# Performance work log

Measured on AMD Instinct MI355X. Metric: run time of the kernel, lower is better.

The kernel has to match this reference:

```python
import jax, jax.numpy as jnp
import numpy as np

B, S, D, V = 64, 128, 64, 50000

def _prelu(x, a):
    return jnp.where(x >= 0, x, a * x)

def setup_inputs() -> dict:
    key = jax.random.key(0)
    ks = jax.random.split(key, 24)
    stdv = 1.0 / np.sqrt(D)
    u = lambda k, shape: jax.random.uniform(k, shape, jnp.float32, -stdv, stdv)
    emb = u(ks[0], (V, D)).at[0].set(0.0)  # padding_idx=0
    inp = {
        'items': jax.random.randint(ks[1], (B, S), 0, V),
        'A': jax.random.randint(ks[2], (B, S, S), 0, 2),
        'edgeorder': jax.random.randint(ks[3], (B, S, S), 0, S),
        'last_nodes': jax.random.randint(ks[4], (B,), 0, S),
        'mask': jnp.ones((B, S), dtype=bool),
        'emb': emb,
        'W_self': u(ks[5], (D, D)), 'W_neigh': u(ks[6], (D, D)),
        'prelu1': jnp.full((D,), 0.25, jnp.float32),
        'Wq': u(ks[7], (D, D)), 'bq': jnp.zeros((D,), jnp.float32),
        'Wk': u(ks[8], (D, D)), 'Wv': u(ks[9], (D, D)), 'we': u(ks[10], (D,)),
        'prelu2': jnp.full((D,), 0.25, jnp.float32),
        'Wu': u(ks[11], (D, D)), 'bu': jnp.zeros((D,), jnp.float32),
        'Wvr': u(ks[12], (D, D)), 'wer': u(ks[13], (D,)),
        'prelu3': jnp.full((D,), 0.25, jnp.float32),
        'W_sr': u(ks[14], (2 * D, D)),
    }
    return inp

def reference(items, A, edgeorder, last_nodes, mask, emb, W_self, W_neigh, prelu1,
              Wq, bq, Wk, Wv, we, prelu2, Wu, bu, Wvr, wer, prelu3, W_sr):
    x = emb[items]  # [B,S,D]
    # ---- EOPA: masked neighbor broadcast + edgeorder gather + max-pool ----
    adjT = (jnp.swapaxes(A, 1, 2) == 1)  # [B,S(target),S(neighbor)]
    neigh = jnp.where((adjT & mask[:, None, :])[..., None], x[:, None, :, :], 0.0)  # [B,S,S,D]
    eo_t = jnp.swapaxes(edgeorder, 1, 2)  # [B,S,S]
    # gathered[b,i,j,:] = neigh[b, edgeorder[b,j,i], j, :]
    neigh = jnp.take_along_axis(neigh, eo_t[..., None], axis=1)
    neigh = neigh.max(axis=2)  # [B,S,D]
    h = _prelu(x @ W_self + neigh @ W_neigh, prelu1)
    # ---- SGAT: sigmoid-gated attention over adjacency ----
    q = h @ Wq + bq
    k = h @ Wk
    v = h @ Wv
    e = k[:, :, None, :] + q[:, None, :, :]             # e[b,i,j,d]
    e = jnp.where((A == 1)[..., None], e, 0.0)
    e = jax.nn.sigmoid(e) @ we                           # [B,S,S]
    a = jax.nn.softmax(e, axis=1)                        # softmax over source i
    h2 = _prelu(jnp.einsum('bij,bid->bjd', a, v), prelu2)
    # ---- AttnReadout ----
    xu = h2 @ Wu + bu                                    # [B,S,D]
    xlast = h2[jnp.arange(h2.shape[0]), last_nodes]      # [B,D]
    xv = xlast @ Wvr
    eatt = jax.nn.sigmoid(xu + xv[:, None, :]) @ wer     # [B,S]
    alpha = jax.nn.softmax(eatt, axis=1)
    out = _prelu((h2 * alpha[..., None]).sum(axis=1), prelu3)  # [B,D]
    # ---- session representation ----
    sr = jnp.concatenate([out, xlast], axis=-1) @ W_sr   # [B,D]
    return sr
```

## Files before the change

### kernel.cpp

```cpp
#include <hip/hip_runtime.h>

#define BB 64
#define SS 128
#define DD 64
#define SSQ (SS*SS)
#define BSD (BB*SS*DD)

__device__ __forceinline__ float fast_sigmoid(float x) {
  return __builtin_amdgcn_rcpf(1.0f + __expf(-x));
}
__device__ __forceinline__ float rl(float v, int l) {
  return __int_as_float(__builtin_amdgcn_readlane(__float_as_int(v), l));
}

__global__ __launch_bounds__(256, 4) void kA(
    const int* __restrict__ items, const int* __restrict__ Aadj,
    const int* __restrict__ eo, const float* __restrict__ emb,
    const float* __restrict__ Wself, const float* __restrict__ Wneigh,
    const float* __restrict__ prelu1,
    const float* __restrict__ Wq, const float* __restrict__ bq,
    const float* __restrict__ Wk, const float* __restrict__ Wv,
    float* __restrict__ q_ws, float* __restrict__ k_ws, float* __restrict__ v_ws)
{
  __shared__ alignas(16) float xs[SS*DD];
  __shared__ unsigned char condw[SS];
  const int b  = blockIdx.x >> 4;
  const int i0 = (blockIdx.x & 15) * 8;
  const int tid = threadIdx.x;
  const int wv = tid >> 6, lane = tid & 63;

  {
    const float4* emb4 = (const float4*)emb;
    float4* xs4 = (float4*)xs;
    for (int f = tid; f < SS*16; f += 256) {
      int j = f >> 4, qd = f & 15;
      xs4[f] = emb4[items[b*SS + j]*16 + qd];
    }
  }
  {
    int eov[4];
#pragma unroll
    for (int kq = 0; kq < 4; kq++) {
      int p = tid + kq*256;
      eov[kq] = eo[b*SSQ + (p >> 3)*SS + i0 + (p & 7)];
    }
#pragma unroll
    for (int kq = 0; kq < 4; kq++) {
      int p = tid + kq*256;
      bool c = (Aadj[b*SSQ + (p >> 3)*SS + eov[kq]] == 1);
      unsigned long long bm = __ballot(c);
      if ((lane & 7) == 0)
        condw[p >> 3] = (unsigned char)(bm >> lane);
    }
  }
  __syncthreads();

  float m[2];
#pragma unroll
  for (int t = 0; t < 2; t++) m[t] = -__builtin_inff();
  for (int j = 0; j < SS; j++) {
    unsigned int cw = (unsigned int)condw[j] >> (wv*2);
    float xv = xs[j*DD + lane];
#pragma unroll
    for (int t = 0; t < 2; t++) {
      float val = ((cw >> t) & 1u) ? xv : 0.0f;
      m[t] = fmaxf(m[t], val);
    }
  }
  float xr[2];
#pragma unroll
  for (int t = 0; t < 2; t++) xr[t] = xs[(i0 + wv*2 + t)*DD + lane];

  float acc[2] = {0.0f, 0.0f};
#pragma unroll 8
  for (int kk = 0; kk < DD; kk++) {
    float w = Wself[kk*DD + lane];
#pragma unroll
    for (int t = 0; t < 2; t++) acc[t] = fmaf(rl(xr[t], kk), w, acc[t]);
  }
#pragma unroll 8
  for (int kk = 0; kk < DD; kk++) {
    float w = Wneigh[kk*DD + lane];
#pragma unroll
    for (int t = 0; t < 2; t++) acc[t] = fmaf(rl(m[t], kk), w, acc[t]);
  }
  float hr[2];
  {
    float p1 = prelu1[lane];
#pragma unroll
    for (int t = 0; t < 2; t++) {
      float h = acc[t];
      hr[t] = (h >= 0.0f) ? h : p1*h;
    }
  }

  const int r0g = b*SS + i0 + wv*2;
  {
    float bqv = bq[lane];
    float a2[2] = {bqv, bqv};
#pragma unroll 8
    for (int kk = 0; kk < DD; kk++) {
      float w = Wq[kk*DD + lane];
#pragma unroll
      for (int t = 0; t < 2; t++) a2[t] = fmaf(rl(hr[t], kk), w, a2[t]);
    }
#pragma unroll
    for (int t = 0; t < 2; t++) q_ws[(r0g + t)*DD + lane] = a2[t];
  }
  {
    float a2[2] = {0.0f, 0.0f};
#pragma unroll 8
    for (int kk = 0; kk < DD; kk++) {
      float w = Wk[kk*DD + lane];
#pragma unroll
      for (int t = 0; t < 2; t++) a2[t] = fmaf(rl(hr[t], kk), w, a2[t]);
    }
#pragma unroll
    for (int t = 0; t < 2; t++) k_ws[(r0g + t)*DD + lane] = a2[t];
  }
  {
    float a2[2] = {0.0f, 0.0f};
#pragma unroll 8
    for (int kk = 0; kk < DD; kk++) {
      float w = Wv[kk*DD + lane];
#pragma unroll
      for (int t = 0; t < 2; t++) a2[t] = fmaf(rl(hr[t], kk), w, a2[t]);
    }
#pragma unroll
    for (int t = 0; t < 2; t++) v_ws[(r0g + t)*DD + lane] = a2[t];
  }
}

__global__ __launch_bounds__(256, 4) void kB(
    const int* __restrict__ Aadj,
    const float* __restrict__ q_ws, const float* __restrict__ k_ws,
    const float* __restrict__ v_ws,
    const float* __restrict__ we, const float* __restrict__ prelu2,
    const float* __restrict__ Wu, const float* __restrict__ bu,
    float* __restrict__ h2_ws, float* __restrict__ xu_ws)
{
  __shared__ alignas(16) float ks[SS*65];
  __shared__ alignas(16) float qs[8*65];
  __shared__ alignas(16) float es[8*129];
  __shared__ float wes[DD];
  const int b  = blockIdx.x >> 4;
  const int j0 = (blockIdx.x & 15) * 8;
  const int tid = threadIdx.x;
  const int wv = tid >> 6, lane = tid & 63;

  {
    const float4* k4 = (const float4*)k_ws;
    for (int f = tid; f < 2048; f += 256) {
      int i = f >> 4, d4 = f & 15;
      float4 v = k4[(b*SS + i)*16 + d4];
      float* dst = &ks[i*65 + d4*4];
      dst[0] = v.x; dst[1] = v.y; dst[2] = v.z; dst[3] = v.w;
    }
    const float4* q4 = (const float4*)q_ws;
    if (tid < 128) {
      int jl = tid >> 4, d4 = tid & 15;
      float4 v = q4[(b*SS + j0 + jl)*16 + d4];
      float* dst = &qs[jl*65 + d4*4];
      dst[0] = v.x; dst[1] = v.y; dst[2] = v.z; dst[3] = v.w;
    }
    if (tid < DD) wes[tid] = we[tid];
  }
  float hw = we[lane];
  for (int off = 32; off >= 1; off >>= 1) hw += __shfl_xor(hw, off);
  const float half_sum = 0.5f * hw;
  __syncthreads();

#pragma unroll
  for (int kq = 0; kq < 4; kq++) {
    int p = tid + kq*256;
    int jl = p & 7, i = p >> 3;
    bool isE = (Aadj[b*SSQ + i*SS + j0 + jl] == 1);
    float s = 0.0f;
    for (int d2 = 0; d2 < DD; d2++) {
      float t = ks[i*65 + d2] + qs[jl*65 + d2];
      s = fmaf(wes[d2], fast_sigmoid(t), s);
    }
    es[jl*129 + i] = isE ? s : half_sum;
  }
  __syncthreads();

  float* vs = ks;
  {
    const float4* v4 = (const float4*)v_ws;
    float4* vs4 = (float4*)vs;
    for (int f = tid; f < 2048; f += 256)
      vs4[f] = v4[b*SS*16 + f];
  }
  float a0n[2], a1n[2];
#pragma unroll
  for (int t = 0; t < 2; t++) {
    int jl = wv*2 + t;
    float a0 = es[jl*129 + lane], a1 = es[jl*129 + 64 + lane];
    float mx = fmaxf(a0, a1);
    for (int off = 32; off >= 1; off >>= 1) mx = fmaxf(mx, __shfl_xor(mx, off));
    float p0 = __expf(a0 - mx), p1 = __expf(a1 - mx);
    float sm = p0 + p1;
    for (int off = 32; off >= 1; off >>= 1) sm += __shfl_xor(sm, off);
    float inv = 1.0f / sm;
    a0n[t] = p0 * inv;
    a1n[t] = p1 * inv;
  }
  __syncthreads();

  float acc[2] = {0.0f, 0.0f};
  for (int i = 0; i < 64; i++) {
    float vv = vs[i*DD + lane];
#pragma unroll
    for (int t = 0; t < 2; t++) acc[t] = fmaf(rl(a0n[t], i), vv, acc[t]);
  }
  for (int i = 0; i < 64; i++) {
    float vv = vs[(64 + i)*DD + lane];
#pragma unroll
    for (int t = 0; t < 2; t++) acc[t] = fmaf(rl(a1n[t], i), vv, acc[t]);
  }
  float h2r[2];
  {
    float p2 = prelu2[lane];
#pragma unroll
    for (int t = 0; t < 2; t++) {
      float h2 = acc[t];
      h2r[t] = (h2 >= 0.0f) ? h2 : p2*h2;
      h2_ws[(b*SS + j0 + wv*2 + t)*DD + lane] = h2r[t];
    }
  }
  {
    float buv = bu[lane];
    float a2[2] = {buv, buv};
#pragma unroll 8
    for (int kk = 0; kk < DD; kk++) {
      float w = Wu[kk*DD + lane];
#pragma unroll
      for (int t = 0; t < 2; t++) a2[t] = fmaf(rl(h2r[t], kk), w, a2[t]);
    }
#pragma unroll
    for (int t = 0; t < 2; t++)
      xu_ws[(b*SS + j0 + wv*2 + t)*DD + lane] = a2[t];
  }
}

__global__ __launch_bounds__(512) void k4_readout(
    const float* __restrict__ h2_ws, const float* __restrict__ xu_ws,
    const int* __restrict__ last_nodes,
    const float* __restrict__ Wvr, const float* __restrict__ wer,
    const float* __restrict__ prelu3, const float* __restrict__ Wsr,
    float* __restrict__ out)
{
  __shared__ float xlast[DD], xv[DD], eatt[SS], alpha[SS], outs[DD];
  __shared__ float pools[8*DD];
  const int b = blockIdx.x;
  const int tid = threadIdx.x;
  const int wv = tid >> 6, lane = tid & 63;

  const int ln = last_nodes[b];
  if (tid < DD) xlast[tid] = h2_ws[(b*SS + ln)*DD + tid];
  __syncthreads();
  {
    float s = 0.0f;
#pragma unroll
    for (int r = 0; r < 8; r++) {
      int k2 = wv*8 + r;
      s = fmaf(xlast[k2], Wvr[k2*DD + lane], s);
    }
    pools[wv*DD + lane] = s;
  }
  __syncthreads();
  if (wv == 0) {
    float s = 0.0f;
#pragma unroll
    for (int w = 0; w < 8; w++) s += pools[w*DD + lane];
    xv[lane] = s;
  }
  __syncthreads();
  {
    float werv = wer[lane];
    float xvl = xv[lane];
    for (int j = wv; j < SS; j += 8) {
      float xuv = xu_ws[(b*SS + j)*DD + lane];
      float term = fast_sigmoid(xuv + xvl) * werv;
      for (int off = 32; off >= 1; off >>= 1) term += __shfl_xor(term, off);
      if (lane == 0) eatt[j] = term;
    }
  }
  __syncthreads();
  if (wv == 0) {
    float a0 = eatt[lane], a1 = eatt[64 + lane];
    float mx = fmaxf(a0, a1);
    for (int off = 32; off >= 1; off >>= 1) mx = fmaxf(mx, __shfl_xor(mx, off));
    float p0 = __expf(a0 - mx), p1 = __expf(a1 - mx);
    float sm = p0 + p1;
    for (int off = 32; off >= 1; off >>= 1) sm += __shfl_xor(sm, off);
    float inv = 1.0f / sm;
    alpha[lane]      = p0 * inv;
    alpha[64 + lane] = p1 * inv;
  }
  __syncthreads();
  {
    float part = 0.0f;
    for (int j = wv; j < SS; j += 8)
      part = fmaf(alpha[j], h2_ws[(b*SS + j)*DD + lane], part);
    pools[wv*DD + lane] = part;
  }
  __syncthreads();
  if (wv == 0) {
    float s = 0.0f;
#pragma unroll
    for (int w = 0; w < 8; w++) s += pools[w*DD + lane];
    float p3 = prelu3[lane];
    outs[lane] = (s >= 0.0f) ? s : p3 * s;
  }
  __syncthreads();
  {
    float fs = 0.0f;
#pragma unroll
    for (int r = 0; r < 16; r++) {
      int m2 = wv*16 + r;
      float src = (m2 < DD) ? outs[m2] : xlast[m2 - DD];
      fs = fmaf(src, Wsr[m2*DD + lane], fs);
    }
    pools[wv*DD + lane] = fs;
  }
  __syncthreads();
  if (wv == 0) {
    float s = 0.0f;
#pragma unroll
    for (int w = 0; w < 8; w++) s += pools[w*DD + lane];
    out[b*DD + lane] = s;
  }
}

extern "C" void kernel_launch(void* const* d_in, const int* in_sizes, int n_in,
                              void* d_out, int out_size, void* d_ws, size_t ws_size,
                              hipStream_t stream)
{
  const int* items = (const int*)d_in[0];
  const int* Aadj  = (const int*)d_in[1];
  const int* eo    = (const int*)d_in[2];
  const int* lastn = (const int*)d_in[3];
  const float* emb    = (const float*)d_in[5];
  const float* Wself  = (const float*)d_in[6];
  const float* Wneigh = (const float*)d_in[7];
  const float* p1     = (const float*)d_in[8];
  const float* Wq     = (const float*)d_in[9];
  const float* bq     = (const float*)d_in[10];
  const float* Wk     = (const float*)d_in[11];
  const float* Wv     = (const float*)d_in[12];
  const float* we     = (const float*)d_in[13];
  const float* p2     = (const float*)d_in[14];
  const float* Wu     = (const float*)d_in[15];
  const float* bu     = (const float*)d_in[16];
  const float* Wvr    = (const float*)d_in[17];
  const float* wer    = (const float*)d_in[18];
  const float* p3     = (const float*)d_in[19];
  const float* Wsr    = (const float*)d_in[20];

  float* ws    = (float*)d_ws;
  float* q_ws  = ws;
  float* k_ws  = ws + (size_t)BSD;
  float* v_ws  = ws + (size_t)2*BSD;
  float* h2_ws = ws + (size_t)3*BSD;
  float* xu_ws = ws + (size_t)4*BSD;

  kA<<<BB*16, 256, 0, stream>>>(items, Aadj, eo, emb, Wself, Wneigh, p1,
                                Wq, bq, Wk, Wv, q_ws, k_ws, v_ws);
  kB<<<BB*16, 256, 0, stream>>>(Aadj, q_ws, k_ws, v_ws, we, p2, Wu, bu,
                                h2_ws, xu_ws);
  k4_readout<<<BB, 512, 0, stream>>>(h2_ws, xu_ws, lastn, Wvr, wer, p3, Wsr,
                                     (float*)d_out);
}
```

Measured before the change: 185.6 us.

## Double rows per block and restructure SGAT edge scoring with transposed K tile

Each block in both kernels now handles 16 rows instead of 8, so the embedding and K/V tiles staged per block are reused twice as much and the grid shrinks to 512 blocks. In kB, K is stored transposed in shared memory, the query lives in registers and is broadcast with readlane, and the adjacency mask is packed into ballot bitmasks. Each lane then computes sigmoid scores for two source nodes across four targets, replacing the per-thread strided dot-product loop and the extra shared-memory score buffer. The trade-off is fewer blocks (about two per CU on a large GPU), higher register pressure with the occupancy hint lowered to 2, and the V load now sitting behind an extra barrier.

Measured after the change: 185.4 us. Within noise of the previous version (-0.2%).

```diff
diff --git a/kernel.cpp b/kernel.cpp
--- a/kernel.cpp
+++ b/kernel.cpp
@@ -13,7 +13,7 @@
   return __int_as_float(__builtin_amdgcn_readlane(__float_as_int(v), l));
 }
 
-__global__ __launch_bounds__(256, 4) void kA(
+__global__ __launch_bounds__(256, 2) void kA(
     const int* __restrict__ items, const int* __restrict__ Aadj,
     const int* __restrict__ eo, const float* __restrict__ emb,
     const float* __restrict__ Wself, const float* __restrict__ Wneigh,
@@ -23,9 +23,9 @@
     float* __restrict__ q_ws, float* __restrict__ k_ws, float* __restrict__ v_ws)
 {
   __shared__ alignas(16) float xs[SS*DD];
-  __shared__ unsigned char condw[SS];
-  const int b  = blockIdx.x >> 4;
-  const int i0 = (blockIdx.x & 15) * 8;
+  __shared__ unsigned short condw[SS];
+  const int b  = blockIdx.x >> 3;
+  const int i0 = (blockIdx.x & 7) * 16;
   const int tid = threadIdx.x;
   const int wv = tid >> 6, lane = tid & 63;
 
@@ -38,100 +38,101 @@
     }
   }
   {
-    int eov[4];
-#pragma unroll
-    for (int kq = 0; kq < 4; kq++) {
+    int eov[8];
+#pragma unroll
+    for (int kq = 0; kq < 8; kq++) {
       int p = tid + kq*256;
-      eov[kq] = eo[b*SSQ + (p >> 3)*SS + i0 + (p & 7)];
-    }
-#pragma unroll
-    for (int kq = 0; kq < 4; kq++) {
+      eov[kq] = eo[b*SSQ + (p >> 4)*SS + i0 + (p & 15)];
+    }
+#pragma unroll
+    for (int kq = 0; kq < 8; kq++) {
       int p = tid + kq*256;
-      bool c = (Aadj[b*SSQ + (p >> 3)*SS + eov[kq]] == 1);
+      bool c = (Aadj[b*SSQ + (p >> 4)*SS + eov[kq]] == 1);
       unsigned long long bm = __ballot(c);
-      if ((lane & 7) == 0)
-        condw[p >> 3] = (unsigned char)(bm >> lane);
-    }
-  }
-  __syncthreads();
-
-  float m[2];
-#pragma unroll
-  for (int t = 0; t < 2; t++) m[t] = -__builtin_inff();
+      if ((lane & 15) == 0)
+        condw[p >> 4] = (unsigned short)(bm >> lane);
+    }
+  }
+  __syncthreads();
+
+  float m[4];
+#pragma unroll
+  for (int t = 0; t < 4; t++) m[t] = -__builtin_inff();
+#pragma unroll 2
   for (int j = 0; j < SS; j++) {
-    unsigned int cw = (unsigned int)condw[j] >> (wv*2);
+    unsigned int cw = (unsigned int)condw[j] >> (wv*4);
     float xv = xs[j*DD + lane];
 #pragma unroll
-    for (int t = 0; t < 2; t++) {
+    for (int t = 0; t < 4; t++) {
       float val = ((cw >> t) & 1u) ? xv : 0.0f;
       m[t] = fmaxf(m[t], val);
     }
   }
-  float xr[2];
-#pragma unroll
-  for (int t = 0; t < 2; t++) xr[t] = xs[(i0 + wv*2 + t)*DD + lane];
-
-  float acc[2] = {0.0f, 0.0f};
+  float xr[4];
+#pragma unroll
+  for (int t = 0; t < 4; t++) xr[t] = xs[(i0 + wv*4 + t)*DD + lane];
+
+  float acc[4] = {0.0f, 0.0f, 0.0f, 0.0f};
 #pragma unroll 8
   for (int kk = 0; kk < DD; kk++) {
     float w = Wself[kk*DD + lane];
 #pragma unroll
-    for (int t = 0; t < 2; t++) acc[t] = fmaf(rl(xr[t], kk), w, acc[t]);
+    for (int t = 0; t < 4; t++) acc[t] = fmaf(rl(xr[t], kk), w, acc[t]);
   }
 #pragma unroll 8
   for (int kk = 0; kk < DD; kk++) {
     float w = Wneigh[kk*DD + lane];
 #pragma unroll
-    for (int t = 0; t < 2; t++) acc[t] = fmaf(rl(m[t], kk), w, acc[t]);
-  }
-  float hr[2];
+    for (int t = 0; t < 4; t++) acc[t] = fmaf(rl(m[t], kk), w, acc[t]);
+  }
+  float hr[4];
   {
     float p1 = prelu1[lane];
 #pragma unroll
-    for (int t = 0; t < 2; t++) {
+    for (int t = 0; t < 4; t++) {
       float h = acc[t];
       hr[t] = (h >= 0.0f) ? h : p1*h;
     }
   }
 
-  const int r0g = b*SS + i0 + wv*2;
+  const int r0g = b*SS + i0 + wv*4;
   {
     float bqv = bq[lane];
-    float a2[2] = {bqv, bqv};
+    float a2[4] = {bqv, bqv, bqv, bqv};
 #pragma unroll 8
     for (int kk = 0; kk < DD; kk++) {
       float w = Wq[kk*DD + lane];
 #pragma unroll
-      for (int t = 0; t < 2; t++) a2[t] = fmaf(rl(hr[t], kk), w, a2[t]);
-    }
-#pragma unroll
-    for (int t = 0; t < 2; t++) q_ws[(r0g + t)*DD + lane] = a2[t];
-  }
-  {
-    float a2[2] = {0.0f, 0.0f};
+      for (int t = 0; t < 4; t++) a2[t] = fmaf(rl(hr[t], kk), w, a2[t]);
+    }
+#pragma unroll
+    for (int t = 0; t < 4; t++) q_ws[(r0g + t)*DD + lane] = a2[t];
+  }
+  {
+    float a2[4] = {0.0f, 0.0f, 0.0f, 0.0f};
 #pragma unroll 8
     for (int kk = 0; kk < DD; kk++) {
       float w = Wk[kk*DD + lane];
 #pragma unroll
-      for (int t = 0; t < 2; t++) a2[t] = fmaf(rl(hr[t], kk), w, a2[t]);
-    }
-#pragma unroll
-    for (int t = 0; t < 2; t++) k_ws[(r0g + t)*DD + lane] = a2[t];
-  }
-  {
-    float a2[2] = {0.0f, 0.0f};
+      for (int t = 0; t < 4; t++) a2[t] = fmaf(rl(hr[t], kk), w, a2[t]);
+    }
+#pragma unroll
+    for (int t = 0; t < 4; t++) k_ws[(r0g + t)*DD + lane] = a2[t];
+  }
+  {
+    float a2[4] = {0.0f, 0.0f, 0.0f, 0.0f};
 #pragma unroll 8
     for (int kk = 0; kk < DD; kk++) {
       float w = Wv[kk*DD + lane];
 #pragma unroll
-      for (int t = 0; t < 2; t++) a2[t] = fmaf(rl(hr[t], kk), w, a2[t]);
-    }
-#pragma unroll
-    for (int t = 0; t < 2; t++) v_ws[(r0g + t)*DD + lane] = a2[t];
-  }
-}
-
-__global__ __launch_bounds__(256, 4) void kB(
+      for (int t = 0; t < 4; t++) a2[t] = fmaf(rl(hr[t], kk), w, a2[t]);
+    }
+#pragma unroll
+    for (int t = 0; t < 4; t++) v_ws[(r0g + t)*DD + lane] = a2[t];
+  }
+}
+
+__global__ __launch_bounds__(256, 2) void kB(
     const int* __restrict__ Aadj,
     const float* __restrict__ q_ws, const float* __restrict__ k_ws,
     const float* __restrict__ v_ws,
@@ -139,66 +140,71 @@
     const float* __restrict__ Wu, const float* __restrict__ bu,
     float* __restrict__ h2_ws, float* __restrict__ xu_ws)
 {
-  __shared__ alignas(16) float ks[SS*65];
-  __shared__ alignas(16) float qs[8*65];
-  __shared__ alignas(16) float es[8*129];
-  __shared__ float wes[DD];
-  const int b  = blockIdx.x >> 4;
-  const int j0 = (blockIdx.x & 15) * 8;
+  __shared__ alignas(16) float kt[DD*129 + 64];
+  __shared__ unsigned long long msk[16*2];
+  const int b  = blockIdx.x >> 3;
+  const int j0 = (blockIdx.x & 7) * 16;
   const int tid = threadIdx.x;
   const int wv = tid >> 6, lane = tid & 63;
 
   {
-    const float4* k4 = (const float4*)k_ws;
+    const float4* k4g = (const float4*)k_ws;
     for (int f = tid; f < 2048; f += 256) {
       int i = f >> 4, d4 = f & 15;
-      float4 v = k4[(b*SS + i)*16 + d4];
-      float* dst = &ks[i*65 + d4*4];
-      dst[0] = v.x; dst[1] = v.y; dst[2] = v.z; dst[3] = v.w;
-    }
-    const float4* q4 = (const float4*)q_ws;
-    if (tid < 128) {
-      int jl = tid >> 4, d4 = tid & 15;
-      float4 v = q4[(b*SS + j0 + jl)*16 + d4];
-      float* dst = &qs[jl*65 + d4*4];
-      dst[0] = v.x; dst[1] = v.y; dst[2] = v.z; dst[3] = v.w;
-    }
-    if (tid < DD) wes[tid] = we[tid];
-  }
-  float hw = we[lane];
+      float4 v = k4g[(b*SS + i)*16 + d4];
+      kt[(4*d4 + 0)*129 + i] = v.x;
+      kt[(4*d4 + 1)*129 + i] = v.y;
+      kt[(4*d4 + 2)*129 + i] = v.z;
+      kt[(4*d4 + 3)*129 + i] = v.w;
+    }
+  }
+  {
+#pragma unroll
+    for (int kq = 0; kq < 8; kq++) {
+      int p = tid + kq*256;
+      int j = p >> 7, i = p & 127;
+      bool c = (Aadj[b*SSQ + i*SS + j0 + j] == 1);
+      unsigned long long bm = __ballot(c);
+      if (lane == 0) msk[j*2 + ((p >> 6) & 1)] = bm;
+    }
+  }
+  float qreg[4];
+#pragma unroll
+  for (int t = 0; t < 4; t++)
+    qreg[t] = q_ws[(b*SS + j0 + wv*4 + t)*DD + lane];
+  float wreg = we[lane];
+  float hw = wreg;
   for (int off = 32; off >= 1; off >>= 1) hw += __shfl_xor(hw, off);
   const float half_sum = 0.5f * hw;
   __syncthreads();
 
-#pragma unroll
-  for (int kq = 0; kq < 4; kq++) {
-    int p = tid + kq*256;
-    int jl = p & 7, i = p >> 3;
-    bool isE = (Aadj[b*SSQ + i*SS + j0 + jl] == 1);
-    float s = 0.0f;
-    for (int d2 = 0; d2 < DD; d2++) {
-      float t = ks[i*65 + d2] + qs[jl*65 + d2];
-      s = fmaf(wes[d2], fast_sigmoid(t), s);
-    }
-    es[jl*129 + i] = isE ? s : half_sum;
-  }
-  __syncthreads();
-
-  float* vs = ks;
-  {
-    const float4* v4 = (const float4*)v_ws;
-    float4* vs4 = (float4*)vs;
-    for (int f = tid; f < 2048; f += 256)
-      vs4[f] = v4[b*SS*16 + f];
-  }
-  float a0n[2], a1n[2];
-#pragma unroll
-  for (int t = 0; t < 2; t++) {
-    int jl = wv*2 + t;
-    float a0 = es[jl*129 + lane], a1 = es[jl*129 + 64 + lane];
-    float mx = fmaxf(a0, a1);
+  unsigned long long mlo[4], mhi[4];
+#pragma unroll
+  for (int t = 0; t < 4; t++) {
+    mlo[t] = msk[(wv*4 + t)*2 + 0];
+    mhi[t] = msk[(wv*4 + t)*2 + 1];
+  }
+
+  float a0[4] = {0,0,0,0}, a1[4] = {0,0,0,0};
+  for (int d = 0; d < DD; d++) {
+    float kd0 = kt[d*129 + lane];
+    float kd1 = kt[d*129 + 64 + lane];
+    float wd = rl(wreg, d);
+#pragma unroll
+    for (int t = 0; t < 4; t++) {
+      float qd = rl(qreg[t], d);
+      a0[t] = fmaf(wd, fast_sigmoid(kd0 + qd), a0[t]);
+      a1[t] = fmaf(wd, fast_sigmoid(kd1 + qd), a1[t]);
+    }
+  }
+  float a0n[4], a1n[4];
+#pragma unroll
+  for (int t = 0; t < 4; t++) {
+    float e0 = ((mlo[t] >> lane) & 1ull) ? a0[t] : half_sum;
+    float e1 = ((mhi[t] >> lane) & 1ull) ? a1[t] : half_sum;
+    float mx = fmaxf(e0, e1);
     for (int off = 32; off >= 1; off >>= 1) mx = fmaxf(mx, __shfl_xor(mx, off));
-    float p0 = __expf(a0 - mx), p1 = __expf(a1 - mx);
+    float p0 = __expf(e0 - mx), p1 = __expf(e1 - mx);
     float sm = p0 + p1;
     for (int off = 32; off >= 1; off >>= 1) sm += __shfl_xor(sm, off);
     float inv = 1.0f / sm;
@@ -207,39 +213,47 @@
   }
   __syncthreads();
 
-  float acc[2] = {0.0f, 0.0f};
+  float* vs = kt;
+  {
+    const float4* v4 = (const float4*)v_ws;
+    float4* vs4 = (float4*)vs;
+    for (int f = tid; f < 2048; f += 256)
+      vs4[f] = v4[b*SS*16 + f];
+  }
+  __syncthreads();
+
+  float acc[4] = {0,0,0,0};
   for (int i = 0; i < 64; i++) {
-    float vv = vs[i*DD + lane];
-#pragma unroll
-    for (int t = 0; t < 2; t++) acc[t] = fmaf(rl(a0n[t], i), vv, acc[t]);
-  }
-  for (int i = 0; i < 64; i++) {
-    float vv = vs[(64 + i)*DD + lane];
-#pragma unroll
-    for (int t = 0; t < 2; t++) acc[t] = fmaf(rl(a1n[t], i), vv, acc[t]);
-  }
-  float h2r[2];
+    float vv0 = vs[i*DD + lane];
+    float vv1 = vs[(64 + i)*DD + lane];
+#pragma unroll
+    for (int t = 0; t < 4; t++) {
+      acc[t] = fmaf(rl(a0n[t], i), vv0, acc[t]);
+      acc[t] = fmaf(rl(a1n[t], i), vv1, acc[t]);
+    }
+  }
+  float h2r[4];
   {
     float p2 = prelu2[lane];
 #pragma unroll
-    for (int t = 0; t < 2; t++) {
+    for (int t = 0; t < 4; t++) {
       float h2 = acc[t];
       h2r[t] = (h2 >= 0.0f) ? h2 : p2*h2;
-      h2_ws[(b*SS + j0 + wv*2 + t)*DD + lane] = h2r[t];
+      h2_ws[(b*SS + j0 + wv*4 + t)*DD + lane] = h2r[t];
     }
   }
   {
     float buv = bu[lane];
-    float a2[2] = {buv, buv};
+    float a2[4] = {buv, buv, buv, buv};
 #pragma unroll 8
     for (int kk = 0; kk < DD; kk++) {
       float w = Wu[kk*DD + lane];
 #pragma unroll
-      for (int t = 0; t < 2; t++) a2[t] = fmaf(rl(h2r[t], kk), w, a2[t]);
-    }
-#pragma unroll
-    for (int t = 0; t < 2; t++)
-      xu_ws[(b*SS + j0 + wv*2 + t)*DD + lane] = a2[t];
+      for (int t = 0; t < 4; t++) a2[t] = fmaf(rl(h2r[t], kk), w, a2[t]);
+    }
+#pragma unroll
+    for (int t = 0; t < 4; t++)
+      xu_ws[(b*SS + j0 + wv*4 + t)*DD + lane] = a2[t];
   }
 }
 
@@ -365,10 +379,10 @@
   float* h2_ws = ws + (size_t)3*BSD;
   float* xu_ws = ws + (size_t)4*BSD;
 
-  kA<<<BB*16, 256, 0, stream>>>(items, Aadj, eo, emb, Wself, Wneigh, p1,
-                                Wq, bq, Wk, Wv, q_ws, k_ws, v_ws);
-  kB<<<BB*16, 256, 0, stream>>>(Aadj, q_ws, k_ws, v_ws, we, p2, Wu, bu,
-                                h2_ws, xu_ws);
+  kA<<<BB*8, 256, 0, stream>>>(items, Aadj, eo, emb, Wself, Wneigh, p1,
+                               Wq, bq, Wk, Wv, q_ws, k_ws, v_ws);
+  kB<<<BB*8, 256, 0, stream>>>(Aadj, q_ws, k_ws, v_ws, we, p2, Wu, bu,
+                               h2_ws, xu_ws);
   k4_readout<<<BB, 512, 0, stream>>>(h2_ws, xu_ws, lastn, Wvr, wer, p3, Wsr,
                                      (float*)d_out);
 }
```
